# Optimization experiments

Hardware: AMD Instinct MI355X
Metric: run time of the kernel (lower is better)

The kernel has to match this reference:

```python
import jax, jax.numpy as jnp
import numpy as np

NUM_HEADS = 4
ALPHA = 0.2  # LeakyReLU negative slope


def setup_inputs() -> dict:
    key = jax.random.key(0)
    k1, k2 = jax.random.split(key)
    input_tensor = jax.random.normal(k1, (2, 4096, 128), dtype=jnp.float32)
    adj_matrix = jax.random.randint(k2, (4096, 4096), 0, 2, dtype=jnp.int32)
    return {"input_tensor": input_tensor, "adj_matrix": adj_matrix}


def reference(input_tensor, adj_matrix):
    B, S, F = input_tensor.shape
    H = NUM_HEADS
    x = input_tensor.reshape(B, S, H, F // H)          # (B,S,H,K)
    # full dense score matrix, QK^T-like with shared projection (identity)
    scores = jnp.einsum('bihk,bjhk->bhij', x, x)        # (B,H,S,S)
    scores = jax.nn.leaky_relu(scores, negative_slope=ALPHA)
    # adjacency mask broadcast over (B,H)
    scores = jnp.where(adj_matrix[None, None, :, :] == 0, -jnp.inf, scores)
    probs = jax.nn.softmax(scores, axis=-1)             # dropout p=0 -> identity
    out = jnp.einsum('bhij,bjhk->bihk', probs, x)       # (B,S,H,K)
    return out.reshape(B, S, F)                          # concat=True
```

## Files before the change

### kernel.cpp

```cpp
#include <hip/hip_runtime.h>
#include <stdint.h>

#define SEQ 4096
#define FDIM 128
#define NH 4
#define HD 32
#define NB 2
#define NROWS (NB * NH * SEQ)
#define LOG2E 1.4426950408889634f
#define NEGBIG (-1.0e30f)

typedef float f32x4 __attribute__((ext_vector_type(4)));
typedef __bf16 bf16x8 __attribute__((ext_vector_type(8)));

__device__ __forceinline__ unsigned short f2bf(float f) {
  unsigned int u = __builtin_bit_cast(unsigned int, f);
  return (unsigned short)((u + 0x7FFFu + ((u >> 16) & 1u)) >> 16);
}

__global__ void cvt_kernel(const float* __restrict__ in, unsigned short* __restrict__ out) {
  int i = (blockIdx.x * 256 + threadIdx.x) * 4;
  float4 v = *reinterpret_cast<const float4*>(in + i);
  ushort4 o;
  o.x = f2bf(v.x); o.y = f2bf(v.y); o.z = f2bf(v.z); o.w = f2bf(v.w);
  *reinterpret_cast<ushort4*>(out + i) = o;
}

__global__ void adjpack_kernel(const int* __restrict__ adj, unsigned short* __restrict__ bits16) {
  size_t t = (size_t)blockIdx.x * 256 + threadIdx.x;
  const uint4* p = reinterpret_cast<const uint4*>(adj) + t * 4;
  uint4 a = p[0], b = p[1], c = p[2], d = p[3];
  unsigned m = 0;
  m |= (a.x != 0) ? 1u : 0u;        m |= (a.y != 0) ? 2u : 0u;
  m |= (a.z != 0) ? 4u : 0u;        m |= (a.w != 0) ? 8u : 0u;
  m |= (b.x != 0) ? 16u : 0u;       m |= (b.y != 0) ? 32u : 0u;
  m |= (b.z != 0) ? 64u : 0u;       m |= (b.w != 0) ? 128u : 0u;
  m |= (c.x != 0) ? 256u : 0u;      m |= (c.y != 0) ? 512u : 0u;
  m |= (c.z != 0) ? 1024u : 0u;     m |= (c.w != 0) ? 2048u : 0u;
  m |= (d.x != 0) ? 4096u : 0u;     m |= (d.y != 0) ? 8192u : 0u;
  m |= (d.z != 0) ? 16384u : 0u;    m |= (d.w != 0) ? 32768u : 0u;
  bits16[t] = (unsigned short)m;
}

template <int NSPLIT>
__global__ __launch_bounds__(256) void gat_kernel(
    const unsigned short* __restrict__ xbf,
    const unsigned long long* __restrict__ bits,
    float* __restrict__ dst,
    float* __restrict__ lbuf) {
  __shared__ __align__(16) unsigned short Kl[64][40];
  __shared__ __align__(16) unsigned Vt32[32 * 38];

  const int bh = blockIdx.y;
  const int b = bh >> 2;
  const int h = bh & 3;
  const int tid = threadIdx.x;
  const int wid = tid >> 6;
  const int lane = tid & 63;
  const int g = lane >> 4;
  const int ql = lane & 15;
  const int qw = blockIdx.x * 64 + wid * 16;
  const int jbase = blockIdx.z * (SEQ / NSPLIT);
  const int NT = (SEQ / NSPLIT) / 64;

  const unsigned short* xb = xbf + ((size_t)b * SEQ) * FDIM + h * HD;

  bf16x8 qraw = __builtin_bit_cast(bf16x8,
      *reinterpret_cast<const uint4*>(xb + (size_t)(qw + ql) * FDIM + g * 8));
  bf16x8 qf;
#pragma unroll
  for (int e = 0; e < 8; ++e) qf[e] = (__bf16)((float)qraw[e] * LOG2E);

  f32x4 acc0 = {0.f, 0.f, 0.f, 0.f};
  f32x4 acc1 = {0.f, 0.f, 0.f, 0.f};
  float lrun = 0.f;

  const unsigned long long* brow = bits + (size_t)(qw + ql) * (SEQ / 64);
  const int bcol0 = jbase >> 6;

  const int pr = tid >> 3;
  const int c4 = tid & 7;
  const unsigned short* s0 = xb + (size_t)(jbase + 2 * pr) * FDIM + c4 * 4;
  const unsigned short* s1 = s0 + FDIM;

  uint2 r0 = *reinterpret_cast<const uint2*>(s0);
  uint2 r1 = *reinterpret_cast<const uint2*>(s1);
  unsigned long long wcur = brow[bcol0];

  for (int t = 0; t < NT; ++t) {
    __syncthreads();
    *reinterpret_cast<uint2*>(&Kl[2 * pr][c4 * 4]) = r0;
    *reinterpret_cast<uint2*>(&Kl[2 * pr + 1][c4 * 4]) = r1;
    {
      unsigned q0 = r0.x, q1 = r0.y, q2 = r1.x, q3 = r1.y;
      Vt32[(c4 * 4 + 0) * 38 + pr] = (q0 & 0xffffu) | (q2 << 16);
      Vt32[(c4 * 4 + 1) * 38 + pr] = (q0 >> 16) | (q2 & 0xffff0000u);
      Vt32[(c4 * 4 + 2) * 38 + pr] = (q1 & 0xffffu) | (q3 << 16);
      Vt32[(c4 * 4 + 3) * 38 + pr] = (q1 >> 16) | (q3 & 0xffff0000u);
    }
    __syncthreads();

    if (t + 1 < NT) {
      s0 += 64 * FDIM;
      s1 += 64 * FDIM;
      r0 = *reinterpret_cast<const uint2*>(s0);
      r1 = *reinterpret_cast<const uint2*>(s1);
    }
    const unsigned long long w64 = wcur;
    if (t + 1 < NT) wcur = brow[bcol0 + t + 1];

    f32x4 sc[4];
#pragma unroll
    for (int t4 = 0; t4 < 4; ++t4) {
      bf16x8 kf = __builtin_bit_cast(bf16x8,
          *reinterpret_cast<const uint4*>(&Kl[t4 * 16 + ql][g * 8]));
      f32x4 z = {0.f, 0.f, 0.f, 0.f};
      sc[t4] = __builtin_amdgcn_mfma_f32_16x16x32_bf16(kf, qf, z, 0, 0, 0);
    }

    const unsigned long long wsh = w64 >> (4 * g);
    const unsigned mlo = (unsigned)wsh;
    const unsigned mhi = (unsigned)(wsh >> 32);
    const unsigned mt[4] = {mlo & 15u, (mlo >> 16) & 15u, mhi & 15u, (mhi >> 16) & 15u};

    float p[4][4];
    float rsum = 0.f;
#pragma unroll
    for (int t4 = 0; t4 < 4; ++t4) {
#pragma unroll
      for (int r = 0; r < 4; ++r) {
        float v = sc[t4][r];
        v = fmaxf(v, 0.2f * v);
        const float e = __builtin_amdgcn_exp2f(v);
        const float pe = (mt[t4] & (1u << r)) ? e : 0.f;
        p[t4][r] = pe;
        rsum += pe;
      }
    }
    lrun += rsum;

    const unsigned short* vbase = reinterpret_cast<const unsigned short*>(Vt32);
#pragma unroll
    for (int u = 0; u < 2; ++u) {
      bf16x8 pa;
#pragma unroll
      for (int tp = 0; tp < 2; ++tp)
#pragma unroll
        for (int r = 0; r < 4; ++r)
          pa[tp * 4 + r] = (__bf16)p[2 * u + tp][r];
#pragma unroll
      for (int cc = 0; cc < 2; ++cc) {
        const unsigned short* vp = vbase + (cc * 16 + ql) * 76 + u * 32 + g * 4;
        uint2 v0 = *reinterpret_cast<const uint2*>(vp);
        uint2 v1 = *reinterpret_cast<const uint2*>(vp + 16);
        uint4 vv = {v0.x, v0.y, v1.x, v1.y};
        bf16x8 vf = __builtin_bit_cast(bf16x8, vv);
        if (cc == 0)
          acc0 = __builtin_amdgcn_mfma_f32_16x16x32_bf16(pa, vf, acc0, 0, 0, 0);
        else
          acc1 = __builtin_amdgcn_mfma_f32_16x16x32_bf16(pa, vf, acc1, 0, 0, 0);
      }
    }
  }

  lrun += __shfl_xor(lrun, 16);
  lrun += __shfl_xor(lrun, 32);

  if (NSPLIT == 1) {
#pragma unroll
    for (int r = 0; r < 4; ++r) {
      const float lr = __shfl(lrun, g * 4 + r);
      const float inv = 1.f / lr;
      const size_t o = ((size_t)b * SEQ + (size_t)(qw + g * 4 + r)) * FDIM + h * HD;
      dst[o + ql] = acc0[r] * inv;
      dst[o + 16 + ql] = acc1[r] * inv;
    }
  } else {
    float* Op = dst + (((size_t)blockIdx.z * (NB * NH) + bh) * SEQ) * HD;
#pragma unroll
    for (int r = 0; r < 4; ++r) {
      const int q = qw + 4 * g + r;
      Op[(size_t)q * HD + ql] = acc0[r];
      Op[(size_t)q * HD + 16 + ql] = acc1[r];
    }
    if (g == 0)
      lbuf[(size_t)blockIdx.z * NROWS + (size_t)bh * SEQ + qw + ql] = lrun;
  }
}

template <int NSPLIT>
__global__ __launch_bounds__(256) void combine_kernel(
    const float* __restrict__ Op, const float* __restrict__ lbuf, float* __restrict__ out) {
  const int idx = blockIdx.x * 256 + threadIdx.x;
  const int row = idx >> 3;
  const int dc = (idx & 7) * 4;
  float lt = 0.f;
  float4 o = {0.f, 0.f, 0.f, 0.f};
#pragma unroll
  for (int s = 0; s < NSPLIT; ++s) {
    lt += lbuf[(size_t)s * NROWS + row];
    float4 v = *reinterpret_cast<const float4*>(
        Op + ((size_t)s * NROWS + row) * HD + dc);
    o.x += v.x; o.y += v.y; o.z += v.z; o.w += v.w;
  }
  const float inv = 1.f / lt;
  const int bh = row >> 12;
  const int q = row & (SEQ - 1);
  const int b = bh >> 2;
  const int h = bh & 3;
  float4 w;
  w.x = o.x * inv; w.y = o.y * inv; w.z = o.z * inv; w.w = o.w * inv;
  *reinterpret_cast<float4*>(out + ((size_t)b * SEQ + q) * FDIM + h * HD + dc) = w;
}

extern "C" void kernel_launch(void* const* d_in, const int* in_sizes, int n_in,
                              void* d_out, int out_size, void* d_ws, size_t ws_size,
                              hipStream_t stream) {
  (void)in_sizes; (void)n_in; (void)out_size;
  const float* x = (const float*)d_in[0];
  const int* adj = (const int*)d_in[1];
  float* outp = (float*)d_out;

  unsigned short* xbf = (unsigned short*)d_ws;
  unsigned short* bits16 = (unsigned short*)((char*)d_ws + (2u << 20));
  float* Opart = (float*)((char*)d_ws + (4u << 20));
  auto need = [](int s) {
    return (size_t)(4u << 20) + (size_t)s * NROWS * HD * 4 + (size_t)s * NROWS * 4;
  };

  cvt_kernel<<<(NB * SEQ * FDIM) / (256 * 4), 256, 0, stream>>>(x, xbf);
  adjpack_kernel<<<(SEQ * SEQ) / (16 * 256), 256, 0, stream>>>(adj, bits16);

  const unsigned long long* bits = (const unsigned long long*)bits16;
  if (ws_size >= need(4)) {
    float* mlb = (float*)((char*)d_ws + (4u << 20) + (size_t)4 * NROWS * HD * 4);
    dim3 grid(SEQ / 64, NB * NH, 4);
    gat_kernel<4><<<grid, 256, 0, stream>>>(xbf, bits, Opart, mlb);
    combine_kernel<4><<<(NROWS * 8) / 256, 256, 0, stream>>>(Opart, mlb, outp);
  } else if (ws_size >= need(2)) {
    float* mlb = (float*)((char*)d_ws + (4u << 20) + (size_t)2 * NROWS * HD * 4);
    dim3 grid(SEQ / 64, NB * NH, 2);
    gat_kernel<2><<<grid, 256, 0, stream>>>(xbf, bits, Opart, mlb);
    combine_kernel<2><<<(NROWS * 8) / 256, 256, 0, stream>>>(Opart, mlb, outp);
  } else {
    dim3 grid(SEQ / 64, NB * NH, 1);
    gat_kernel<1><<<grid, 256, 0, stream>>>(xbf, bits, outp, nullptr);
  }
}
```

Baseline: 75.14 us.

## Repack V tile for 16-byte LDS reads and compute row sums via MFMA

```diff
diff --git a/kernel.cpp b/kernel.cpp
--- a/kernel.cpp
+++ b/kernel.cpp
@@ -8,7 +8,6 @@
 #define NB 2
 #define NROWS (NB * NH * SEQ)
 #define LOG2E 1.4426950408889634f
-#define NEGBIG (-1.0e30f)
 
 typedef float f32x4 __attribute__((ext_vector_type(4)));
 typedef __bf16 bf16x8 __attribute__((ext_vector_type(8)));
@@ -43,13 +42,13 @@
 }
 
 template <int NSPLIT>
-__global__ __launch_bounds__(256) void gat_kernel(
+__global__ __launch_bounds__(256, 4) void gat_kernel(
     const unsigned short* __restrict__ xbf,
     const unsigned long long* __restrict__ bits,
     float* __restrict__ dst,
     float* __restrict__ lbuf) {
   __shared__ __align__(16) unsigned short Kl[64][40];
-  __shared__ __align__(16) unsigned Vt32[32 * 38];
+  __shared__ __align__(16) unsigned short Vp[32 * 72];
 
   const int bh = blockIdx.y;
   const int b = bh >> 2;
@@ -71,9 +70,13 @@
 #pragma unroll
   for (int e = 0; e < 8; ++e) qf[e] = (__bf16)((float)qraw[e] * LOG2E);
 
+  bf16x8 ones;
+#pragma unroll
+  for (int e = 0; e < 8; ++e) ones[e] = (__bf16)1.0f;
+
   f32x4 acc0 = {0.f, 0.f, 0.f, 0.f};
   f32x4 acc1 = {0.f, 0.f, 0.f, 0.f};
-  float lrun = 0.f;
+  f32x4 accL = {0.f, 0.f, 0.f, 0.f};
 
   const unsigned long long* brow = bits + (size_t)(qw + ql) * (SEQ / 64);
   const int bcol0 = jbase >> 6;
@@ -81,30 +84,31 @@
   const int pr = tid >> 3;
   const int c4 = tid & 7;
   const unsigned short* s0 = xb + (size_t)(jbase + 2 * pr) * FDIM + c4 * 4;
-  const unsigned short* s1 = s0 + FDIM;
+
+  const int pi0h = (32 * (pr >> 4) + 8 * ((pr >> 1) & 3) + 4 * ((pr >> 3) & 1) + 2 * (pr & 1)) >> 1;
+  unsigned* vw = reinterpret_cast<unsigned*>(Vp) + pi0h;
 
   uint2 r0 = *reinterpret_cast<const uint2*>(s0);
-  uint2 r1 = *reinterpret_cast<const uint2*>(s1);
+  uint2 r1 = *reinterpret_cast<const uint2*>(s0 + FDIM);
   unsigned long long wcur = brow[bcol0];
+
+  const unsigned selA = 0x05040100u;
+  const unsigned selB = 0x07060302u;
 
   for (int t = 0; t < NT; ++t) {
     __syncthreads();
     *reinterpret_cast<uint2*>(&Kl[2 * pr][c4 * 4]) = r0;
     *reinterpret_cast<uint2*>(&Kl[2 * pr + 1][c4 * 4]) = r1;
-    {
-      unsigned q0 = r0.x, q1 = r0.y, q2 = r1.x, q3 = r1.y;
-      Vt32[(c4 * 4 + 0) * 38 + pr] = (q0 & 0xffffu) | (q2 << 16);
-      Vt32[(c4 * 4 + 1) * 38 + pr] = (q0 >> 16) | (q2 & 0xffff0000u);
-      Vt32[(c4 * 4 + 2) * 38 + pr] = (q1 & 0xffffu) | (q3 << 16);
-      Vt32[(c4 * 4 + 3) * 38 + pr] = (q1 >> 16) | (q3 & 0xffff0000u);
-    }
+    vw[(4 * c4 + 0) * 36] = __builtin_amdgcn_perm(r1.x, r0.x, selA);
+    vw[(4 * c4 + 1) * 36] = __builtin_amdgcn_perm(r1.x, r0.x, selB);
+    vw[(4 * c4 + 2) * 36] = __builtin_amdgcn_perm(r1.y, r0.y, selA);
+    vw[(4 * c4 + 3) * 36] = __builtin_amdgcn_perm(r1.y, r0.y, selB);
     __syncthreads();
 
     if (t + 1 < NT) {
       s0 += 64 * FDIM;
-      s1 += 64 * FDIM;
       r0 = *reinterpret_cast<const uint2*>(s0);
-      r1 = *reinterpret_cast<const uint2*>(s1);
+      r1 = *reinterpret_cast<const uint2*>(s0 + FDIM);
     }
     const unsigned long long w64 = wcur;
     if (t + 1 < NT) wcur = brow[bcol0 + t + 1];
@@ -119,27 +123,23 @@
     }
 
     const unsigned long long wsh = w64 >> (4 * g);
-    const unsigned mlo = (unsigned)wsh;
-    const unsigned mhi = (unsigned)(wsh >> 32);
-    const unsigned mt[4] = {mlo & 15u, (mlo >> 16) & 15u, mhi & 15u, (mhi >> 16) & 15u};
-
-    float p[4][4];
-    float rsum = 0.f;
+    const unsigned mw[2] = {(unsigned)wsh, (unsigned)(wsh >> 32)};
+
+    float pf[4][4];
 #pragma unroll
     for (int t4 = 0; t4 < 4; ++t4) {
+      const unsigned word = mw[t4 >> 1];
 #pragma unroll
       for (int r = 0; r < 4; ++r) {
         float v = sc[t4][r];
         v = fmaxf(v, 0.2f * v);
-        const float e = __builtin_amdgcn_exp2f(v);
-        const float pe = (mt[t4] & (1u << r)) ? e : 0.f;
-        p[t4][r] = pe;
-        rsum += pe;
+        float e = __builtin_amdgcn_exp2f(v);
+        const int pos = 16 * (t4 & 1) + r;
+        const unsigned msk = (unsigned)((int)(word << (31 - pos)) >> 31);
+        pf[t4][r] = __builtin_bit_cast(float, __builtin_bit_cast(unsigned, e) & msk);
       }
     }
-    lrun += rsum;
-
-    const unsigned short* vbase = reinterpret_cast<const unsigned short*>(Vt32);
+
 #pragma unroll
     for (int u = 0; u < 2; ++u) {
       bf16x8 pa;
@@ -147,31 +147,22 @@
       for (int tp = 0; tp < 2; ++tp)
 #pragma unroll
         for (int r = 0; r < 4; ++r)
-          pa[tp * 4 + r] = (__bf16)p[2 * u + tp][r];
-#pragma unroll
-      for (int cc = 0; cc < 2; ++cc) {
-        const unsigned short* vp = vbase + (cc * 16 + ql) * 76 + u * 32 + g * 4;
-        uint2 v0 = *reinterpret_cast<const uint2*>(vp);
-        uint2 v1 = *reinterpret_cast<const uint2*>(vp + 16);
-        uint4 vv = {v0.x, v0.y, v1.x, v1.y};
-        bf16x8 vf = __builtin_bit_cast(bf16x8, vv);
-        if (cc == 0)
-          acc0 = __builtin_amdgcn_mfma_f32_16x16x32_bf16(pa, vf, acc0, 0, 0, 0);
-        else
-          acc1 = __builtin_amdgcn_mfma_f32_16x16x32_bf16(pa, vf, acc1, 0, 0, 0);
-      }
-    }
-  }
-
-  lrun += __shfl_xor(lrun, 16);
-  lrun += __shfl_xor(lrun, 32);
+          pa[tp * 4 + r] = (__bf16)pf[2 * u + tp][r];
+      bf16x8 vf0 = __builtin_bit_cast(bf16x8,
+          *reinterpret_cast<const uint4*>(&Vp[ql * 72 + u * 32 + g * 8]));
+      bf16x8 vf1 = __builtin_bit_cast(bf16x8,
+          *reinterpret_cast<const uint4*>(&Vp[(16 + ql) * 72 + u * 32 + g * 8]));
+      acc0 = __builtin_amdgcn_mfma_f32_16x16x32_bf16(pa, vf0, acc0, 0, 0, 0);
+      acc1 = __builtin_amdgcn_mfma_f32_16x16x32_bf16(pa, vf1, acc1, 0, 0, 0);
+      accL = __builtin_amdgcn_mfma_f32_16x16x32_bf16(pa, ones, accL, 0, 0, 0);
+    }
+  }
 
   if (NSPLIT == 1) {
 #pragma unroll
     for (int r = 0; r < 4; ++r) {
-      const float lr = __shfl(lrun, g * 4 + r);
-      const float inv = 1.f / lr;
-      const size_t o = ((size_t)b * SEQ + (size_t)(qw + g * 4 + r)) * FDIM + h * HD;
+      const float inv = 1.f / accL[r];
+      const size_t o = ((size_t)b * SEQ + (size_t)(qw + 4 * g + r)) * FDIM + h * HD;
       dst[o + ql] = acc0[r] * inv;
       dst[o + 16 + ql] = acc1[r] * inv;
     }
@@ -183,8 +174,11 @@
       Op[(size_t)q * HD + ql] = acc0[r];
       Op[(size_t)q * HD + 16 + ql] = acc1[r];
     }
-    if (g == 0)
-      lbuf[(size_t)blockIdx.z * NROWS + (size_t)bh * SEQ + qw + ql] = lrun;
+    if (ql == 0) {
+#pragma unroll
+      for (int r = 0; r < 4; ++r)
+        lbuf[(size_t)blockIdx.z * NROWS + (size_t)bh * SEQ + qw + 4 * g + r] = accL[r];
+    }
   }
 }
 
```

New measurement: 72.45 us. 3.6% less time.
